# Performance work log

Hardware: AMD Instinct MI355X
Metric: run time of the kernel (lower is better)

The kernel has to match this reference:

```python
import jax, jax.numpy as jnp
import numpy as np

N, E, G = 50000, 640000, 256
NODE_IN, EDGE_IN, EXT_IN = 32, 16, 8
H, L = 128, 3
BN_EPS = 1e-5


def _linear_init(key, fan_in, fan_out):
    kw, kb = jax.random.split(key)
    s = 1.0 / np.sqrt(fan_in)
    w = jax.random.uniform(kw, (fan_in, fan_out), minval=-s, maxval=s, dtype=jnp.float32)
    b = jax.random.uniform(kb, (fan_out,), minval=-s, maxval=s, dtype=jnp.float32)
    return w, b


def setup_inputs() -> dict:
    key = jax.random.key(0)
    ks = jax.random.split(key, 16)
    x = jax.random.normal(ks[0], (N, NODE_IN), dtype=jnp.float32)
    edge_index = jax.random.randint(ks[1], (2, E), 0, N)
    edge_attr = jax.random.normal(ks[2], (E, EDGE_IN), dtype=jnp.float32)
    batch = jnp.sort(jax.random.randint(ks[3], (N,), 0, G))
    externals = jax.random.normal(ks[4], (G, EXT_IN), dtype=jnp.float32)

    node_w, node_b = _linear_init(ks[5], NODE_IN, H)
    ee_w1, ee_b1 = _linear_init(ks[6], EDGE_IN, H)
    ee_w2, ee_b2 = _linear_init(ks[7], H, H)
    # stacked per-layer GINEConv MLP params: [L, H, H] / [L, H]
    cks = jax.random.split(ks[8], 2 * L)
    cw1, cb1, cw2, cb2 = [], [], [], []
    for l in range(L):
        w1, b1 = _linear_init(cks[2 * l], H, H)
        w2, b2 = _linear_init(cks[2 * l + 1], H, H)
        cw1.append(w1); cb1.append(b1); cw2.append(w2); cb2.append(b2)
    conv_w1 = jnp.stack(cw1); conv_b1 = jnp.stack(cb1)
    conv_w2 = jnp.stack(cw2); conv_b2 = jnp.stack(cb2)
    bn_gamma = jnp.ones((L, H), dtype=jnp.float32)
    bn_beta = jnp.zeros((L, H), dtype=jnp.float32)
    ext_w1, ext_b1 = _linear_init(ks[9], EXT_IN, H)
    ext_w2, ext_b2 = _linear_init(ks[10], H, H)
    reg_w1, reg_b1 = _linear_init(ks[11], 2 * H, H)
    reg_w2, reg_b2 = _linear_init(ks[12], H, 1)

    return dict(x=x, edge_attr=edge_attr, externals=externals,
                node_w=node_w, node_b=node_b,
                ee_w1=ee_w1, ee_b1=ee_b1, ee_w2=ee_w2, ee_b2=ee_b2,
                conv_w1=conv_w1, conv_b1=conv_b1, conv_w2=conv_w2, conv_b2=conv_b2,
                bn_gamma=bn_gamma, bn_beta=bn_beta,
                ext_w1=ext_w1, ext_b1=ext_b1, ext_w2=ext_w2, ext_b2=ext_b2,
                reg_w1=reg_w1, reg_b1=reg_b1, reg_w2=reg_w2, reg_b2=reg_b2,
                edge_index=edge_index, batch=batch, num_graphs=G)


def reference(x, edge_attr, externals,
              node_w, node_b, ee_w1, ee_b1, ee_w2, ee_b2,
              conv_w1, conv_b1, conv_w2, conv_b2, bn_gamma, bn_beta,
              ext_w1, ext_b1, ext_w2, ext_b2,
              reg_w1, reg_b1, reg_w2, reg_b2,
              edge_index, batch, num_graphs):
    n = x.shape[0]
    src, dst = edge_index[0], edge_index[1]
    h = x @ node_w + node_b                                      # [N,H]
    e = jax.nn.relu(edge_attr @ ee_w1 + ee_b1) @ ee_w2 + ee_b2   # [E,H]
    for l in range(conv_w1.shape[0]):
        # GINEConv (eps=0): aggr = sum_j relu(x_j + e_ij); out = MLP(x_i + aggr)
        msg = jax.nn.relu(h[src] + e)                            # gather + add + relu [E,H]
        aggr = jax.ops.segment_sum(msg, dst, num_segments=n)     # scatter-add [N,H]
        z = h + aggr
        z = jax.nn.relu(z @ conv_w1[l] + conv_b1[l]) @ conv_w2[l] + conv_b2[l]
        # BatchNorm1d (batch statistics)
        mean = z.mean(axis=0)
        var = z.var(axis=0)
        z = (z - mean) * jax.lax.rsqrt(var + BN_EPS) * bn_gamma[l] + bn_beta[l]
        h = jax.nn.relu(z)                                       # dropout = identity (eval)
    # global mean pool over graphs
    gsum = jax.ops.segment_sum(h, batch, num_segments=num_graphs)
    cnt = jax.ops.segment_sum(jnp.ones((n, 1), h.dtype), batch, num_segments=num_graphs)
    graph_emb = gsum / jnp.maximum(cnt, 1.0)
    ext = jax.nn.relu(externals @ ext_w1 + ext_b1) @ ext_w2 + ext_b2
    comb = jnp.concatenate([graph_emb, ext], axis=-1)            # [G,2H]
    out = jax.nn.relu(comb @ reg_w1 + reg_b1) @ reg_w2 + reg_b2  # [G,1]
    return out.squeeze(-1)
```

## Files before the change

kernel.cpp:

```cpp
#include <hip/hip_runtime.h>

typedef __bf16 bf16_t;
typedef __bf16 bf16x8 __attribute__((ext_vector_type(8)));
typedef __bf16 bf16x4 __attribute__((ext_vector_type(4)));
typedef __bf16 bf16x2 __attribute__((ext_vector_type(2)));
typedef float  f32x4  __attribute__((ext_vector_type(4)));

#define MFMA16(a, b, c) __builtin_amdgcn_mfma_f32_16x16x32_bf16((a), (b), (c), 0, 0, 0)

__global__ __launch_bounds__(256) void prep_all_kernel(
    const float* __restrict__ nw,  const float* __restrict__ ew1,
    const float* __restrict__ ew2, const float* __restrict__ cw1,
    const float* __restrict__ cw2,
    bf16_t* __restrict__ nwt,  bf16_t* __restrict__ ew1t,
    bf16_t* __restrict__ ew2t, bf16_t* __restrict__ cw1t,
    bf16_t* __restrict__ cw2t)
{
    int b = blockIdx.x;
    const float* W; bf16_t* O; int Kact, KP, lb;
    if (b < 16)       { W = nw;  O = nwt;  Kact = 32;  KP = 32;  lb = b; }
    else if (b < 32)  { W = ew1; O = ew1t; Kact = 16;  KP = 32;  lb = b - 16; }
    else if (b < 96)  { W = ew2; O = ew2t; Kact = 128; KP = 128; lb = b - 32; }
    else if (b < 288) { int l = (b - 96) / 64;  W = cw1 + l * 16384; O = cw1t + l * 16384;
                        Kact = 128; KP = 128; lb = (b - 96) % 64; }
    else              { int l = (b - 288) / 64; W = cw2 + l * 16384; O = cw2t + l * 16384;
                        Kact = 128; KP = 128; lb = (b - 288) % 64; }
    int idx = lb * 256 + threadIdx.x;
    if (idx >= 128 * KP) return;
    int j    = idx & 7;
    int lane = (idx >> 3) & 63;
    int ct   = (idx >> 9) & 7;
    int kc   = idx >> 12;
    int n = ct * 16 + (lane & 15);
    int k = kc * 32 + (lane >> 4) * 8 + j;
    O[idx] = (bf16_t)((k < Kact) ? W[k * 128 + n] : 0.0f);
}

__global__ __launch_bounds__(256) void hist_kernel(const int* __restrict__ ei,
                                                   int* __restrict__ deg, int E,
                                                   const float* __restrict__ ea) {
    int t = blockIdx.x * 256 + threadIdx.x;
    if (t < E) {
        atomicAdd(&deg[ei[(long)E + t]], 1);
        float w0 = ea[(long)t * 16];
        float w1 = ea[(long)t * 16 + 8];
        asm volatile("" :: "v"(w0), "v"(w1));
    }
}

__global__ __launch_bounds__(256) void scanA_kernel(const int* __restrict__ deg,
                                                    int* __restrict__ partials,
                                                    int* __restrict__ bsums, int N) {
    __shared__ int s[256];
    int b = blockIdx.x, t = threadIdx.x;
    int base = b * 1024 + t * 4;
    int v0 = (base + 0 < N) ? deg[base + 0] : 0;
    int v1 = (base + 1 < N) ? deg[base + 1] : 0;
    int v2 = (base + 2 < N) ? deg[base + 2] : 0;
    int v3 = (base + 3 < N) ? deg[base + 3] : 0;
    int local = v0 + v1 + v2 + v3;
    s[t] = local;
    __syncthreads();
    for (int off = 1; off < 256; off <<= 1) {
        int v = (t >= off) ? s[t - off] : 0;
        __syncthreads();
        s[t] += v;
        __syncthreads();
    }
    int excl = s[t] - local;
    if (base + 0 < N) partials[base + 0] = excl;
    if (base + 1 < N) partials[base + 1] = excl + v0;
    if (base + 2 < N) partials[base + 2] = excl + v0 + v1;
    if (base + 3 < N) partials[base + 3] = excl + v0 + v1 + v2;
    if (t == 255) bsums[b] = s[255];
}

__global__ __launch_bounds__(256) void scanB_kernel(const int* __restrict__ bsums,
                                                    int* __restrict__ boff,
                                                    int* __restrict__ rowptr,
                                                    int NB, int N) {
    __shared__ int s[256];
    int t = threadIdx.x;
    int local = (t < NB) ? bsums[t] : 0;
    s[t] = local;
    __syncthreads();
    for (int off = 1; off < 256; off <<= 1) {
        int v = (t >= off) ? s[t - off] : 0;
        __syncthreads();
        s[t] += v;
        __syncthreads();
    }
    if (t < NB) boff[t] = s[t] - local;
    if (t == NB - 1) rowptr[N] = s[t];
}

__global__ __launch_bounds__(256) void scanC_kernel(const int* __restrict__ partials,
                                                    const int* __restrict__ boff,
                                                    int* __restrict__ rowptr,
                                                    int* __restrict__ cursor, int N) {
    int i = blockIdx.x * 256 + threadIdx.x;
    if (i >= N) return;
    int v = partials[i] + boff[i >> 10];
    rowptr[i] = v;
    cursor[i] = v;
}

__global__ __launch_bounds__(256) void scatter_kernel(const int* __restrict__ ei,
                                                      int* __restrict__ cursor,
                                                      int* __restrict__ srcp,
                                                      int* __restrict__ eorig, int E) {
    int t = blockIdx.x * 256 + threadIdx.x;
    if (t >= E) return;
    int d = ei[(long)E + t];
    int pos = atomicAdd(&cursor[d], 1);
    srcp[pos] = ei[t];
    eorig[pos] = t;
}

__global__ __launch_bounds__(256) void node_enc_kernel(
    const float* __restrict__ A, int M,
    const bf16_t* __restrict__ Ws, const float* __restrict__ bias,
    bf16_t* __restrict__ outp)
{
    constexpr int S = 136;
    __shared__ bf16_t T[128 * S];

    const int  tid  = threadIdx.x;
    const int  wv   = tid >> 6, lane = tid & 63;
    const long row0 = (long)blockIdx.x * 128;
    const int  l16  = lane & 15, quad = lane >> 4;

    {
        int r  = wv * 32 + (lane >> 1);
        long gr = row0 + r;
        int c0 = (lane & 1) * 16;
#pragma unroll
        for (int q = 0; q < 4; ++q) {
            float4 v = make_float4(0.f, 0.f, 0.f, 0.f);
            if (gr < M) v = *(const float4*)(A + gr * 32 + c0 + q * 4);
            bf16_t* d = &T[r * S + c0 + q * 4];
            d[0] = (bf16_t)v.x; d[1] = (bf16_t)v.y; d[2] = (bf16_t)v.z; d[3] = (bf16_t)v.w;
        }
    }

    f32x4 acc[2][8];
#pragma unroll
    for (int r = 0; r < 2; r++)
#pragma unroll
        for (int c = 0; c < 8; c++) acc[r][c] = (f32x4){0.f, 0.f, 0.f, 0.f};

    {
        bf16x8 af0 = *(const bf16x8*)&T[(wv * 32 + l16) * S + quad * 8];
        bf16x8 af1 = *(const bf16x8*)&T[(wv * 32 + 16 + l16) * S + quad * 8];
#pragma unroll
        for (int c = 0; c < 8; c++) {
            bf16x8 bfr = *(const bf16x8*)&Ws[((c * 64) + lane) * 8];
            acc[0][c] = MFMA16(af0, bfr, acc[0][c]);
            acc[1][c] = MFMA16(af1, bfr, acc[1][c]);
        }
    }

#pragma unroll
    for (int r = 0; r < 2; r++) {
        int mrow = wv * 32 + r * 16 + quad * 4;
#pragma unroll
        for (int c = 0; c < 8; c++) {
            int col = c * 16 + l16;
            float bb = bias[col];
#pragma unroll
            for (int q = 0; q < 4; q++)
                T[(mrow + q) * S + col] = (bf16_t)(acc[r][c][q] + bb);
        }
    }

#pragma unroll
    for (int it = 0; it < 8; ++it) {
        int idx = it * 64 + lane;
        int row = wv * 32 + (idx >> 4);
        int seg = idx & 15;
        long grow = row0 + row;
        if (grow < M)
            *(uint4*)&outp[grow * 128 + seg * 8] = *(const uint4*)&T[row * S + seg * 8];
    }
}

__global__ __launch_bounds__(256) void edge_mlp_kernel(
    const float* __restrict__ A, int M,
    const bf16_t* __restrict__ Ws1, const float* __restrict__ b1,
    const bf16_t* __restrict__ Ws2, const float* __restrict__ b2,
    const int* __restrict__ eorig, bf16_t* __restrict__ outp)
{
    constexpr int S = 136;
    __shared__ bf16_t T[64 * S];

    const int  tid  = threadIdx.x;
    const int  wv   = tid >> 6, lane = tid & 63;
    const long row0 = (long)blockIdx.x * 64;
    const int  l16  = lane & 15, quad = lane >> 4;

    {
        int  r  = wv * 16 + (lane >> 2);
        long gr = row0 + r;
        float4 v = make_float4(0.f, 0.f, 0.f, 0.f);
        if (gr < M) {
            long eo = eorig[gr];
            v = *(const float4*)(A + eo * 16 + (lane & 3) * 4);
        }
        bf16_t* d = &T[r * S + (lane & 3) * 4];
        d[0] = (bf16_t)v.x; d[1] = (bf16_t)v.y; d[2] = (bf16_t)v.z; d[3] = (bf16_t)v.w;
    }

    f32x4 acc[8];
#pragma unroll
    for (int c = 0; c < 8; c++) acc[c] = (f32x4){0.f, 0.f, 0.f, 0.f};

    {
        bf16x8 af;
#pragma unroll
        for (int j = 0; j < 8; ++j) af[j] = (bf16_t)0.f;
        if (quad < 2) af = *(const bf16x8*)&T[(wv * 16 + l16) * S + quad * 8];
#pragma unroll
        for (int c = 0; c < 8; c++) {
            bf16x8 bfr = *(const bf16x8*)&Ws1[((c * 64) + lane) * 8];
            acc[c] = MFMA16(af, bfr, acc[c]);
        }
    }

    const int mbase = wv * 16 + quad * 4;

#pragma unroll
    for (int c = 0; c < 8; c++) {
        int col = c * 16 + l16;
        float bb = b1[col];
#pragma unroll
        for (int q = 0; q < 4; q++)
            T[(mbase + q) * S + col] = (bf16_t)fmaxf(acc[c][q] + bb, 0.f);
    }

#pragma unroll
    for (int c = 0; c < 8; c++) acc[c] = (f32x4){0.f, 0.f, 0.f, 0.f};

#pragma unroll
    for (int kc = 0; kc < 4; ++kc) {
        bf16x8 af = *(const bf16x8*)&T[(wv * 16 + l16) * S + kc * 32 + quad * 8];
#pragma unroll
        for (int c = 0; c < 8; c++) {
            bf16x8 bfr = *(const bf16x8*)&Ws2[(((kc * 8 + c) * 64) + lane) * 8];
            acc[c] = MFMA16(af, bfr, acc[c]);
        }
    }

#pragma unroll
    for (int c = 0; c < 8; c++) {
        int col = c * 16 + l16;
        float bb = b2[col];
#pragma unroll
        for (int q = 0; q < 4; q++)
            T[(mbase + q) * S + col] = (bf16_t)(acc[c][q] + bb);
    }

#pragma unroll
    for (int it = 0; it < 4; ++it) {
        int idx = it * 64 + lane;
        int row = wv * 16 + (idx >> 4);
        int seg = idx & 15;
        long grow = row0 + row;
        if (grow < M)
            *(uint4*)&outp[grow * 128 + seg * 8] = *(const uint4*)&T[row * S + seg * 8];
    }
}

__global__ __launch_bounds__(256) void bnx_kernel(
    const bf16_t* __restrict__ z, const float* __restrict__ bns,
    const float* __restrict__ gamma, const float* __restrict__ beta,
    bf16_t* __restrict__ hbuf, int N)
{
    long t = (long)blockIdx.x * 256 + threadIdx.x;
    long i0 = t * 8;
    if (i0 >= (long)N * 128) return;
    int c = (int)(i0 & 127);
    const float invN = 1.f / (float)N;
    bf16x8 v = *(const bf16x8*)(z + i0);
    bf16x8 o;
#pragma unroll
    for (int u = 0; u < 8; ++u) {
        int cc = c + u;
        float m  = bns[cc] * invN;
        float va = bns[128 + cc] * invN - m * m;
        float iv = rsqrtf(va + 1e-5f);
        float sc = gamma[cc] * iv;
        float sh = beta[cc] - m * sc;
        o[u] = (bf16_t)fmaxf((float)v[u] * sc + sh, 0.f);
    }
    *(bf16x8*)(hbuf + i0) = o;
}

__global__ __launch_bounds__(512) void aggr_conv_kernel(
    const bf16_t* __restrict__ xin,
    const bf16_t* __restrict__ e,
    const int* __restrict__ rowptr, const int* __restrict__ srcp, int M,
    const bf16_t* __restrict__ Ws1, const float* __restrict__ b1,
    const bf16_t* __restrict__ Ws2, const float* __restrict__ b2,
    bf16_t* __restrict__ zout, float* __restrict__ bn_out)
{
    constexpr int S = 136;
    __shared__ bf16_t T[64 * S];

    const int  tid  = threadIdx.x;
    const int  wv   = tid >> 6, lane = tid & 63;
    const int  tw   = wv >> 1, sub = wv & 1;
    const int  l16  = lane & 15, quad = lane >> 4;
    const long row0 = (long)blockIdx.x * 64;

    const long nbase = row0 + tw * 16 + sub * 8;
    int rpv = 0;
    {
        long idx = nbase + lane;
        if (idx > M) idx = M;
        if (lane <= 8) rpv = rowptr[idx];
    }

#pragma unroll 1
    for (int r8 = 0; r8 < 8; ++r8) {
        const int  r   = tw * 16 + sub * 8 + r8;
        const long n   = row0 + r;
        const int  beg = __shfl(rpv, r8);
        const int  end = __shfl(rpv, r8 + 1);
        float a[8];
#pragma unroll
        for (int u = 0; u < 8; ++u) a[u] = 0.f;
        if (n < M) {
            for (int base = beg; base < end; base += 64) {
                int cnt = min(64, end - base);
                int sv  = (base + lane < end) ? srcp[base + lane] : 0;
                int ng  = (cnt + 3) >> 2;
                for (int jj = 0; jj < ng; ++jj) {
                    int  ei = jj * 4 + quad;
                    bool vv = ei < cnt;
                    int  ec = vv ? ei : (cnt - 1);
                    int  src = __shfl(sv, ec);
                    bf16x8 xv = *(const bf16x8*)(xin + (long)src * 128 + l16 * 8);
                    bf16x8 ev = *(const bf16x8*)(e + (long)(base + ec) * 128 + l16 * 8);
#pragma unroll
                    for (int u = 0; u < 8; ++u) {
                        float t = fmaxf((float)xv[u] + (float)ev[u], 0.f);
                        a[u] += vv ? t : 0.f;
                    }
                }
            }
#pragma unroll
            for (int u = 0; u < 8; ++u) {
                a[u] += __shfl_xor(a[u], 16);
                a[u] += __shfl_xor(a[u], 32);
            }
            bf16x8 xs = *(const bf16x8*)(xin + n * 128 + l16 * 8);
#pragma unroll
            for (int u = 0; u < 8; ++u) a[u] += (float)xs[u];
        }
        if (quad == 0) {
            bf16x8 o;
#pragma unroll
            for (int u = 0; u < 8; ++u) o[u] = (bf16_t)a[u];
            *(uint4*)&T[r * S + l16 * 8] = *(uint4*)&o;
        }
    }
    __syncthreads();

    if (sub == 0) {
        const int mbase = tw * 16 + quad * 4;

        f32x4 acc[8];
#pragma unroll
        for (int c = 0; c < 8; c++) acc[c] = (f32x4){0.f, 0.f, 0.f, 0.f};

#pragma unroll
        for (int kc = 0; kc < 4; ++kc) {
            bf16x8 af = *(const bf16x8*)&T[(tw * 16 + l16) * S + kc * 32 + quad * 8];
#pragma unroll
            for (int c = 0; c < 8; c++) {
                bf16x8 bfr = *(const bf16x8*)&Ws1[(((kc * 8 + c) * 64) + lane) * 8];
                acc[c] = MFMA16(af, bfr, acc[c]);
            }
        }

#pragma unroll
        for (int c = 0; c < 8; c++) {
            int col = c * 16 + l16;
            float bb = b1[col];
#pragma unroll
            for (int q = 0; q < 4; q++)
                T[(mbase + q) * S + col] = (bf16_t)fmaxf(acc[c][q] + bb, 0.f);
        }

#pragma unroll
        for (int c = 0; c < 8; c++) acc[c] = (f32x4){0.f, 0.f, 0.f, 0.f};

#pragma unroll
        for (int kc = 0; kc < 4; ++kc) {
            bf16x8 af = *(const bf16x8*)&T[(tw * 16 + l16) * S + kc * 32 + quad * 8];
#pragma unroll
            for (int c = 0; c < 8; c++) {
                bf16x8 bfr = *(const bf16x8*)&Ws2[(((kc * 8 + c) * 64) + lane) * 8];
                acc[c] = MFMA16(af, bfr, acc[c]);
            }
        }

        float ssum[8], ssq[8];
#pragma unroll
        for (int c = 0; c < 8; c++) {
            int col = c * 16 + l16;
            float bb = b2[col];
            float s = 0.f, s2 = 0.f;
#pragma unroll
            for (int q = 0; q < 4; q++) {
                float v = acc[c][q] + bb;
                T[(mbase + q) * S + col] = (bf16_t)v;
                if (row0 + mbase + q < M) { s += v; s2 += v * v; }
            }
            s  += __shfl_xor(s, 16);  s  += __shfl_xor(s, 32);
            s2 += __shfl_xor(s2, 16); s2 += __shfl_xor(s2, 32);
            ssum[c] = s; ssq[c] = s2;
        }

#pragma unroll
        for (int it = 0; it < 4; ++it) {
            int idx = it * 64 + lane;
            int row = tw * 16 + (idx >> 4);
            int seg = idx & 15;
            long grow = row0 + row;
            if (grow < M)
                *(uint4*)&zout[grow * 128 + seg * 8] = *(const uint4*)&T[row * S + seg * 8];
        }

        float* wred = (float*)&T[(size_t)(tw * 16) * S];
        if (quad == 0) {
#pragma unroll
            for (int c = 0; c < 8; c++) {
                int col = c * 16 + l16;
                wred[col]       = ssum[c];
                wred[128 + col] = ssq[c];
            }
        }
    }
    __syncthreads();
    if (tid < 128) {
        float s = 0.f, s2 = 0.f;
#pragma unroll
        for (int w = 0; w < 4; ++w) {
            const float* wr = (const float*)&T[(size_t)(w * 16) * S];
            s  += wr[tid];
            s2 += wr[128 + tid];
        }
        atomicAdd(&bn_out[tid], s);
        atomicAdd(&bn_out[128 + tid], s2);
    }
}

__global__ __launch_bounds__(128) void pool_kernel(
    const bf16_t* __restrict__ z, const float* __restrict__ bns,
    const float* __restrict__ gamma, const float* __restrict__ beta,
    const int* __restrict__ batch,
    float* __restrict__ gsum, float* __restrict__ cnt, int N)
{
    int c = threadIdx.x;
    float mean = bns[c] / (float)N;
    float var  = bns[128 + c] / (float)N - mean * mean;
    float inv  = rsqrtf(var + 1e-5f);
    float sc   = gamma[c] * inv;
    float sh   = beta[c] - mean * sc;
    int n0 = blockIdx.x * 32;
    int n1 = min(n0 + 32, N);
    float acc = 0.f;
    int cur = -1, rc = 0;
    for (int n = n0; n < n1; ++n) {
        int g = batch[n];
        if (g != cur) {
            if (cur >= 0) {
                atomicAdd(&gsum[(long)cur * 128 + c], acc);
                if (c == 0) atomicAdd(&cnt[cur], (float)rc);
            }
            cur = g; acc = 0.f; rc = 0;
        }
        acc += fmaxf((float)z[(long)n * 128 + c] * sc + sh, 0.f);
        rc++;
    }
    if (cur >= 0) {
        atomicAdd(&gsum[(long)cur * 128 + c], acc);
        if (c == 0) atomicAdd(&cnt[cur], (float)rc);
    }
}

__global__ __launch_bounds__(128) void head_kernel(
    const float* __restrict__ gsum, const float* __restrict__ cnt,
    const float* __restrict__ ext_in,
    const float* __restrict__ ew1, const float* __restrict__ eb1,
    const float* __restrict__ ew2, const float* __restrict__ eb2,
    const float* __restrict__ rw1, const float* __restrict__ rb1,
    const float* __restrict__ rw2, const float* __restrict__ rb2,
    float* __restrict__ out)
{
    int g = blockIdx.x, c = threadIdx.x;
    __shared__ float sx[8];
    __shared__ float h1[128];
    __shared__ float comb[256];
    __shared__ float red[128];

    if (c < 8) sx[c] = ext_in[g * 8 + c];
    __syncthreads();
    float a = eb1[c];
#pragma unroll
    for (int k = 0; k < 8; k++) a += sx[k] * ew1[k * 128 + c];
    h1[c] = fmaxf(a, 0.f);
    __syncthreads();
    float b = eb2[c];
    for (int k = 0; k < 128; k++) b += h1[k] * ew2[k * 128 + c];
    comb[c]       = gsum[(long)g * 128 + c] / fmaxf(cnt[g], 1.0f);
    comb[128 + c] = b;
    __syncthreads();
    float r = rb1[c];
    for (int k = 0; k < 256; k++) r += comb[k] * rw1[k * 128 + c];
    r = fmaxf(r, 0.f);
    red[c] = r * rw2[c];
    __syncthreads();
    if (c == 0) {
        float s = rb2[0];
        for (int k = 0; k < 128; k++) s += red[k];
        out[g] = s;
    }
}

extern "C" void kernel_launch(void* const* d_in, const int* in_sizes, int n_in,
                              void* d_out, int out_size, void* d_ws, size_t ws_size,
                              hipStream_t stream)
{
    const float* x         = (const float*)d_in[0];
    const float* edge_attr = (const float*)d_in[1];
    const float* externals = (const float*)d_in[2];
    const float* node_w    = (const float*)d_in[3];
    const float* node_b    = (const float*)d_in[4];
    const float* ee_w1     = (const float*)d_in[5];
    const float* ee_b1     = (const float*)d_in[6];
    const float* ee_w2     = (const float*)d_in[7];
    const float* ee_b2     = (const float*)d_in[8];
    const float* conv_w1   = (const float*)d_in[9];
    const float* conv_b1   = (const float*)d_in[10];
    const float* conv_w2   = (const float*)d_in[11];
    const float* conv_b2   = (const float*)d_in[12];
    const float* bn_gamma  = (const float*)d_in[13];
    const float* bn_beta   = (const float*)d_in[14];
    const float* ext_w1    = (const float*)d_in[15];
    const float* ext_b1    = (const float*)d_in[16];
    const float* ext_w2    = (const float*)d_in[17];
    const float* ext_b2    = (const float*)d_in[18];
    const float* reg_w1    = (const float*)d_in[19];
    const float* reg_b1    = (const float*)d_in[20];
    const float* reg_w2    = (const float*)d_in[21];
    const float* reg_b2    = (const float*)d_in[22];
    const int* edge_index  = (const int*)d_in[23];
    const int* batch       = (const int*)d_in[24];

    const int N = in_sizes[0] / 32;
    const int E = in_sizes[1] / 16;
    const int G = in_sizes[2] / 8;
    const int NB = (N + 1023) / 1024;

    char* p = (char*)d_ws;
    auto alloc = [&](size_t bytes) -> void* {
        void* r = (void*)p;
        p += (bytes + 255) & ~(size_t)255;
        return r;
    };
    bf16_t* h       = (bf16_t*)alloc((size_t)N * 128 * 2);
    bf16_t* zA      = (bf16_t*)alloc((size_t)N * 128 * 2);
    bf16_t* zB      = (bf16_t*)alloc((size_t)N * 128 * 2);
    bf16_t* hb      = (bf16_t*)alloc((size_t)N * 128 * 2);
    bf16_t* ebuf    = (bf16_t*)alloc((size_t)E * 128 * 2);
    int*    deg     = (int*)alloc((size_t)N * 4);
    int*    rowptr  = (int*)alloc(((size_t)N + 1) * 4);
    int*    cursor  = (int*)alloc((size_t)N * 4);
    int*    partials= (int*)alloc((size_t)N * 4);
    int*    bsums   = (int*)alloc((size_t)NB * 4);
    int*    boff    = (int*)alloc((size_t)NB * 4);
    int*    srcp    = (int*)alloc((size_t)E * 4);
    int*    eorig   = (int*)alloc((size_t)E * 4);
    bf16_t* node_wt = (bf16_t*)alloc(128 * 32 * 2);
    bf16_t* ee_w1t  = (bf16_t*)alloc(128 * 32 * 2);
    bf16_t* ee_w2t  = (bf16_t*)alloc(128 * 128 * 2);
    bf16_t* cw1t    = (bf16_t*)alloc(3 * 128 * 128 * 2);
    bf16_t* cw2t    = (bf16_t*)alloc(3 * 128 * 128 * 2);
    float*  bns     = (float*)alloc(3 * 256 * 4);
    float*  gsum    = (float*)alloc((size_t)G * 128 * 4);
    float*  cnt     = (float*)alloc((size_t)G * 4);

    hipMemsetAsync(deg, 0, (size_t)N * 4, stream);
    hipMemsetAsync(bns, 0, 3 * 256 * 4, stream);
    hist_kernel<<<(E + 255) / 256, 256, 0, stream>>>(edge_index, deg, E, edge_attr);
    scanA_kernel<<<NB, 256, 0, stream>>>(deg, partials, bsums, N);
    scanB_kernel<<<1, 256, 0, stream>>>(bsums, boff, rowptr, NB, N);
    scanC_kernel<<<(N + 255) / 256, 256, 0, stream>>>(partials, boff, rowptr, cursor, N);
    scatter_kernel<<<(E + 255) / 256, 256, 0, stream>>>(edge_index, cursor, srcp, eorig, E);

    prep_all_kernel<<<480, 256, 0, stream>>>(node_w, ee_w1, ee_w2, conv_w1, conv_w2,
                                             node_wt, ee_w1t, ee_w2t, cw1t, cw2t);

    node_enc_kernel<<<(N + 127) / 128, 256, 0, stream>>>(x, N, node_wt, node_b, h);

    edge_mlp_kernel<<<(E + 63) / 64, 256, 0, stream>>>(
        edge_attr, E, ee_w1t, ee_b1, ee_w2t, ee_b2, eorig, ebuf);

    const int nblk = (N + 63) / 64;
    const int bblk = ((N * 128 / 8) + 255) / 256;
    aggr_conv_kernel<<<nblk, 512, 0, stream>>>(
        h, ebuf, rowptr, srcp, N,
        cw1t + 0 * 16384, conv_b1 + 0 * 128, cw2t + 0 * 16384, conv_b2 + 0 * 128,
        zA, bns + 0);
    bnx_kernel<<<bblk, 256, 0, stream>>>(zA, bns + 0, bn_gamma + 0, bn_beta + 0, hb, N);
    aggr_conv_kernel<<<nblk, 512, 0, stream>>>(
        hb, ebuf, rowptr, srcp, N,
        cw1t + 1 * 16384, conv_b1 + 1 * 128, cw2t + 1 * 16384, conv_b2 + 1 * 128,
        zB, bns + 256);
    bnx_kernel<<<bblk, 256, 0, stream>>>(zB, bns + 256, bn_gamma + 128, bn_beta + 128, hb, N);
    aggr_conv_kernel<<<nblk, 512, 0, stream>>>(
        hb, ebuf, rowptr, srcp, N,
        cw1t + 2 * 16384, conv_b1 + 2 * 128, cw2t + 2 * 16384, conv_b2 + 2 * 128,
        zA, bns + 512);

    hipMemsetAsync(gsum, 0, (size_t)G * 128 * 4, stream);
    hipMemsetAsync(cnt, 0, (size_t)G * 4, stream);
    pool_kernel<<<(N + 31) / 32, 128, 0, stream>>>(zA, bns + 512, bn_gamma + 256, bn_beta + 256,
                                                   batch, gsum, cnt, N);
    head_kernel<<<G, 128, 0, stream>>>(gsum, cnt, externals,
                                       ext_w1, ext_b1, ext_w2, ext_b2,
                                       reg_w1, reg_b1, reg_w2, reg_b2,
                                       (float*)d_out);
}
```

Measured before the change: 612.8 us.

## Restructure aggr_conv to 32-row tiles with all waves sharing gather and MFMA work

Each block now handles 32 nodes instead of 64. Each wave gathers neighbour features for 4 nodes, with one whole wavefront per node reading 2 channels per lane and unrolling 4 edges at a time, replacing the older layout where quads handled different edges. All 8 waves now take part in the two 128x128 MFMA stages by splitting column tiles, where before only half of them did. The BN partial sums move to a dedicated shared buffer. The changes aim to raise occupancy (launch bounds 512,8) and stop half the waves idling during the GEMMs. In exchange the kernel adds more __syncthreads and issues narrower 4-byte loads per lane.

```diff
diff --git a/kernel.cpp b/kernel.cpp
--- a/kernel.cpp
+++ b/kernel.cpp
@@ -295,7 +295,7 @@
     *(bf16x8*)(hbuf + i0) = o;
 }
 
-__global__ __launch_bounds__(512) void aggr_conv_kernel(
+__global__ __launch_bounds__(512, 8) void aggr_conv_kernel(
     const bf16_t* __restrict__ xin,
     const bf16_t* __restrict__ e,
     const int* __restrict__ rowptr, const int* __restrict__ srcp, int M,
@@ -304,155 +304,143 @@
     bf16_t* __restrict__ zout, float* __restrict__ bn_out)
 {
     constexpr int S = 136;
-    __shared__ bf16_t T[64 * S];
+    __shared__ bf16_t T[32 * S];
+    __shared__ float  wred[2][256];
 
     const int  tid  = threadIdx.x;
     const int  wv   = tid >> 6, lane = tid & 63;
-    const int  tw   = wv >> 1, sub = wv & 1;
+    const long row0 = (long)blockIdx.x * 32;
     const int  l16  = lane & 15, quad = lane >> 4;
-    const long row0 = (long)blockIdx.x * 64;
-
-    const long nbase = row0 + tw * 16 + sub * 8;
+
+    const long nbase = row0 + wv * 4;
     int rpv = 0;
     {
         long idx = nbase + lane;
         if (idx > M) idx = M;
-        if (lane <= 8) rpv = rowptr[idx];
+        if (lane <= 4) rpv = rowptr[idx];
     }
 
 #pragma unroll 1
-    for (int r8 = 0; r8 < 8; ++r8) {
-        const int  r   = tw * 16 + sub * 8 + r8;
+    for (int ri = 0; ri < 4; ++ri) {
+        const int  r   = wv * 4 + ri;
         const long n   = row0 + r;
-        const int  beg = __shfl(rpv, r8);
-        const int  end = __shfl(rpv, r8 + 1);
-        float a[8];
-#pragma unroll
-        for (int u = 0; u < 8; ++u) a[u] = 0.f;
+        const int  beg = __shfl(rpv, ri);
+        const int  end = __shfl(rpv, ri + 1);
+        float ax = 0.f, ay = 0.f;
         if (n < M) {
+            bf16x2 xv = *(const bf16x2*)(xin + n * 128 + lane * 2);
+            ax = (float)xv[0]; ay = (float)xv[1];
             for (int base = beg; base < end; base += 64) {
                 int cnt = min(64, end - base);
                 int sv  = (base + lane < end) ? srcp[base + lane] : 0;
-                int ng  = (cnt + 3) >> 2;
-                for (int jj = 0; jj < ng; ++jj) {
-                    int  ei = jj * 4 + quad;
-                    bool vv = ei < cnt;
-                    int  ec = vv ? ei : (cnt - 1);
-                    int  src = __shfl(sv, ec);
-                    bf16x8 xv = *(const bf16x8*)(xin + (long)src * 128 + l16 * 8);
-                    bf16x8 ev = *(const bf16x8*)(e + (long)(base + ec) * 128 + l16 * 8);
-#pragma unroll
-                    for (int u = 0; u < 8; ++u) {
-                        float t = fmaxf((float)xv[u] + (float)ev[u], 0.f);
-                        a[u] += vv ? t : 0.f;
-                    }
+                int j = 0;
+                for (; j + 3 < cnt; j += 4) {
+                    int s0 = __shfl(sv, j),     s1 = __shfl(sv, j + 1);
+                    int s2 = __shfl(sv, j + 2), s3 = __shfl(sv, j + 3);
+                    bf16x2 x0 = *(const bf16x2*)(xin + (long)s0 * 128 + lane * 2);
+                    bf16x2 x1 = *(const bf16x2*)(xin + (long)s1 * 128 + lane * 2);
+                    bf16x2 x2 = *(const bf16x2*)(xin + (long)s2 * 128 + lane * 2);
+                    bf16x2 x3 = *(const bf16x2*)(xin + (long)s3 * 128 + lane * 2);
+                    bf16x2 e0 = *(const bf16x2*)(e + (long)(base + j + 0) * 128 + lane * 2);
+                    bf16x2 e1 = *(const bf16x2*)(e + (long)(base + j + 1) * 128 + lane * 2);
+                    bf16x2 e2 = *(const bf16x2*)(e + (long)(base + j + 2) * 128 + lane * 2);
+                    bf16x2 e3 = *(const bf16x2*)(e + (long)(base + j + 3) * 128 + lane * 2);
+                    ax += fmaxf((float)x0[0] + (float)e0[0], 0.f);
+                    ay += fmaxf((float)x0[1] + (float)e0[1], 0.f);
+                    ax += fmaxf((float)x1[0] + (float)e1[0], 0.f);
+                    ay += fmaxf((float)x1[1] + (float)e1[1], 0.f);
+                    ax += fmaxf((float)x2[0] + (float)e2[0], 0.f);
+                    ay += fmaxf((float)x2[1] + (float)e2[1], 0.f);
+                    ax += fmaxf((float)x3[0] + (float)e3[0], 0.f);
+                    ay += fmaxf((float)x3[1] + (float)e3[1], 0.f);
+                }
+                for (; j < cnt; ++j) {
+                    int s0 = __shfl(sv, j);
+                    bf16x2 x0 = *(const bf16x2*)(xin + (long)s0 * 128 + lane * 2);
+                    bf16x2 e0 = *(const bf16x2*)(e + (long)(base + j) * 128 + lane * 2);
+                    ax += fmaxf((float)x0[0] + (float)e0[0], 0.f);
+                    ay += fmaxf((float)x0[1] + (float)e0[1], 0.f);
                 }
             }
-#pragma unroll
-            for (int u = 0; u < 8; ++u) {
-                a[u] += __shfl_xor(a[u], 16);
-                a[u] += __shfl_xor(a[u], 32);
-            }
-            bf16x8 xs = *(const bf16x8*)(xin + n * 128 + l16 * 8);
-#pragma unroll
-            for (int u = 0; u < 8; ++u) a[u] += (float)xs[u];
-        }
+        }
+        bf16x2 o; o[0] = (bf16_t)ax; o[1] = (bf16_t)ay;
+        *(bf16x2*)&T[r * S + lane * 2] = o;
+    }
+    __syncthreads();
+
+    const int rb = wv >> 2, cq = wv & 3;
+    const int mbase = rb * 16 + quad * 4;
+
+    f32x4 acc[2];
+#pragma unroll
+    for (int c = 0; c < 2; c++) acc[c] = (f32x4){0.f, 0.f, 0.f, 0.f};
+
+#pragma unroll
+    for (int kc = 0; kc < 4; ++kc) {
+        bf16x8 af = *(const bf16x8*)&T[(rb * 16 + l16) * S + kc * 32 + quad * 8];
+#pragma unroll
+        for (int c = 0; c < 2; c++) {
+            int ct = cq * 2 + c;
+            bf16x8 bfr = *(const bf16x8*)&Ws1[(((kc * 8 + ct) * 64) + lane) * 8];
+            acc[c] = MFMA16(af, bfr, acc[c]);
+        }
+    }
+    __syncthreads();
+
+#pragma unroll
+    for (int c = 0; c < 2; c++) {
+        int col = (cq * 2 + c) * 16 + l16;
+        float bb = b1[col];
+#pragma unroll
+        for (int q = 0; q < 4; q++)
+            T[(mbase + q) * S + col] = (bf16_t)fmaxf(acc[c][q] + bb, 0.f);
+    }
+    __syncthreads();
+
+#pragma unroll
+    for (int c = 0; c < 2; c++) acc[c] = (f32x4){0.f, 0.f, 0.f, 0.f};
+
+#pragma unroll
+    for (int kc = 0; kc < 4; ++kc) {
+        bf16x8 af = *(const bf16x8*)&T[(rb * 16 + l16) * S + kc * 32 + quad * 8];
+#pragma unroll
+        for (int c = 0; c < 2; c++) {
+            int ct = cq * 2 + c;
+            bf16x8 bfr = *(const bf16x8*)&Ws2[(((kc * 8 + ct) * 64) + lane) * 8];
+            acc[c] = MFMA16(af, bfr, acc[c]);
+        }
+    }
+    __syncthreads();
+
+#pragma unroll
+    for (int c = 0; c < 2; c++) {
+        int col = (cq * 2 + c) * 16 + l16;
+        float bb = b2[col];
+        float s = 0.f, s2 = 0.f;
+#pragma unroll
+        for (int q = 0; q < 4; q++) {
+            float v = acc[c][q] + bb;
+            T[(mbase + q) * S + col] = (bf16_t)v;
+            if (row0 + mbase + q < M) { s += v; s2 += v * v; }
+        }
+        s  += __shfl_xor(s, 16);  s  += __shfl_xor(s, 32);
+        s2 += __shfl_xor(s2, 16); s2 += __shfl_xor(s2, 32);
         if (quad == 0) {
-            bf16x8 o;
-#pragma unroll
-            for (int u = 0; u < 8; ++u) o[u] = (bf16_t)a[u];
-            *(uint4*)&T[r * S + l16 * 8] = *(uint4*)&o;
-        }
-    }
-    __syncthreads();
-
-    if (sub == 0) {
-        const int mbase = tw * 16 + quad * 4;
-
-        f32x4 acc[8];
-#pragma unroll
-        for (int c = 0; c < 8; c++) acc[c] = (f32x4){0.f, 0.f, 0.f, 0.f};
-
-#pragma unroll
-        for (int kc = 0; kc < 4; ++kc) {
-            bf16x8 af = *(const bf16x8*)&T[(tw * 16 + l16) * S + kc * 32 + quad * 8];
-#pragma unroll
-            for (int c = 0; c < 8; c++) {
-                bf16x8 bfr = *(const bf16x8*)&Ws1[(((kc * 8 + c) * 64) + lane) * 8];
-                acc[c] = MFMA16(af, bfr, acc[c]);
-            }
-        }
-
-#pragma unroll
-        for (int c = 0; c < 8; c++) {
-            int col = c * 16 + l16;
-            float bb = b1[col];
-#pragma unroll
-            for (int q = 0; q < 4; q++)
-                T[(mbase + q) * S + col] = (bf16_t)fmaxf(acc[c][q] + bb, 0.f);
-        }
-
-#pragma unroll
-        for (int c = 0; c < 8; c++) acc[c] = (f32x4){0.f, 0.f, 0.f, 0.f};
-
-#pragma unroll
-        for (int kc = 0; kc < 4; ++kc) {
-            bf16x8 af = *(const bf16x8*)&T[(tw * 16 + l16) * S + kc * 32 + quad * 8];
-#pragma unroll
-            for (int c = 0; c < 8; c++) {
-                bf16x8 bfr = *(const bf16x8*)&Ws2[(((kc * 8 + c) * 64) + lane) * 8];
-                acc[c] = MFMA16(af, bfr, acc[c]);
-            }
-        }
-
-        float ssum[8], ssq[8];
-#pragma unroll
-        for (int c = 0; c < 8; c++) {
-            int col = c * 16 + l16;
-            float bb = b2[col];
-            float s = 0.f, s2 = 0.f;
-#pragma unroll
-            for (int q = 0; q < 4; q++) {
-                float v = acc[c][q] + bb;
-                T[(mbase + q) * S + col] = (bf16_t)v;
-                if (row0 + mbase + q < M) { s += v; s2 += v * v; }
-            }
-            s  += __shfl_xor(s, 16);  s  += __shfl_xor(s, 32);
-            s2 += __shfl_xor(s2, 16); s2 += __shfl_xor(s2, 32);
-            ssum[c] = s; ssq[c] = s2;
-        }
-
-#pragma unroll
-        for (int it = 0; it < 4; ++it) {
-            int idx = it * 64 + lane;
-            int row = tw * 16 + (idx >> 4);
-            int seg = idx & 15;
-            long grow = row0 + row;
-            if (grow < M)
-                *(uint4*)&zout[grow * 128 + seg * 8] = *(const uint4*)&T[row * S + seg * 8];
-        }
-
-        float* wred = (float*)&T[(size_t)(tw * 16) * S];
-        if (quad == 0) {
-#pragma unroll
-            for (int c = 0; c < 8; c++) {
-                int col = c * 16 + l16;
-                wred[col]       = ssum[c];
-                wred[128 + col] = ssq[c];
-            }
-        }
-    }
-    __syncthreads();
-    if (tid < 128) {
-        float s = 0.f, s2 = 0.f;
-#pragma unroll
-        for (int w = 0; w < 4; ++w) {
-            const float* wr = (const float*)&T[(size_t)(w * 16) * S];
-            s  += wr[tid];
-            s2 += wr[128 + tid];
-        }
-        atomicAdd(&bn_out[tid], s);
-        atomicAdd(&bn_out[128 + tid], s2);
+            wred[rb][col]       = s;
+            wred[rb][128 + col] = s2;
+        }
+    }
+    __syncthreads();
+
+    {
+        int row = tid >> 4, seg = tid & 15;
+        long grow = row0 + row;
+        if (grow < M)
+            *(uint4*)&zout[grow * 128 + seg * 8] = *(const uint4*)&T[row * S + seg * 8];
+    }
+    if (tid < 256) {
+        float v = wred[0][tid] + wred[1][tid];
+        atomicAdd(&bn_out[tid], v);
     }
 }
 
@@ -608,7 +596,7 @@
     edge_mlp_kernel<<<(E + 63) / 64, 256, 0, stream>>>(
         edge_attr, E, ee_w1t, ee_b1, ee_w2t, ee_b2, eorig, ebuf);
 
-    const int nblk = (N + 63) / 64;
+    const int nblk = (N + 31) / 32;
     const int bblk = ((N * 128 / 8) + 255) / 256;
     aggr_conv_kernel<<<nblk, 512, 0, stream>>>(
         h, ebuf, rowptr, srcp, N,
```

Result: faster. 563.3 us (-8.1%).
